# Performance work log

Measured on AMD Instinct MI355X. Metric: run time of the kernel, lower is better.

The kernel has to match this reference:

```python
import jax, jax.numpy as jnp
import numpy as np

L, T, F = 16, 262144, 2
N = 524288
HIDDEN, OUT = 64, 3
_b = np.exp((np.log(64.0) - np.log(16.0)) / (L - 1))
# per-level resolutions: floor(N_min * b**l), kept as float for the scale multiply
N_VALUES = np.floor(np.float32(16.0 * _b ** np.arange(L))).astype(np.float32)


def setup_inputs() -> dict:
    key = jax.random.key(0)
    ks = jax.random.split(key, 6)
    X = jax.random.uniform(ks[0], (N, 2), jnp.float32)
    hash_table = jax.random.uniform(ks[1], (L, T, F), jnp.float32, minval=-1e-4, maxval=1e-4)

    def lin(k, fan_in, fan_out):
        kw, kb = jax.random.split(k)
        bound = 1.0 / np.sqrt(fan_in)
        W = jax.random.uniform(kw, (fan_in, fan_out), jnp.float32, minval=-bound, maxval=bound)
        b = jax.random.uniform(kb, (fan_out,), jnp.float32, minval=-bound, maxval=bound)
        return W, b

    W1, b1 = lin(ks[2], L * F, HIDDEN)
    W2, b2 = lin(ks[3], HIDDEN, HIDDEN)
    W3, b3 = lin(ks[4], HIDDEN, HIDDEN)
    W4, b4 = lin(ks[5], HIDDEN, OUT)
    return dict(X=X, hash_table=hash_table, W1=W1, b1=b1, W2=W2, b2=b2,
                W3=W3, b3=b3, W4=W4, b4=b4)


def _encode(X, hash_table):
    nvals = jnp.asarray(N_VALUES)
    x_scaled = X[:, :, None] * nvals                      # [N,2,L]
    frac = x_scaled - jnp.floor(x_scaled)                 # [N,2,L]
    vertices = jnp.array([[0., 0., 1., 1.], [0., 1., 0., 1.]], jnp.float32)  # [2,4]
    # faithful to source: scaled coord * vertex mask (not floor + offset), then int truncation
    x_vert = (x_scaled[:, :, :, None] * vertices[None, :, None, :]).astype(jnp.uint32)  # [N,2,L,4]
    primes = jnp.array([1, 2654435761], dtype=jnp.uint32)
    xt = x_vert * primes[None, :, None, None]
    # source takes xor then mod 2 (not mod T); LSB is exact under uint32 wraparound
    x_hash = (jnp.bitwise_xor(xt[:, 0], xt[:, 1]) % 2).astype(jnp.int32)  # [N,L,4] in {0,1}
    xp = jnp.transpose(x_hash, (1, 0, 2))                 # [L,N,4]
    # faithful to source's torch.gather along dim 0: out[l,n,k,f] = table[hash, k, f]
    lookup = hash_table[xp, jnp.arange(4)[None, None, :], :]  # [L,N,4,F]
    lookup = jnp.transpose(lookup, (1, 0, 2, 3))          # [N,L,4,F]
    fx, fy = frac[:, 0, :], frac[:, 1, :]
    cx, cy = 1.0 - fx, 1.0 - fy
    f_stack = jnp.stack([cx * cy, cx * fy, fx * cy, fx * fy], axis=2)  # [N,L,4]
    x_interp = jnp.einsum('nlv,nlvf->nlf', f_stack, lookup)           # [N,L,F]
    return x_interp.reshape(-1, L * F)


def reference(X, hash_table, W1, b1, W2, b2, W3, b3, W4, b4):
    h = _encode(X, hash_table)
    lrelu = lambda z: jnp.where(z >= 0, z, 0.01 * z)  # LeakyReLU default slope
    h = lrelu(h @ W1 + b1)
    h = lrelu(h @ W2 + b2)
    h = lrelu(h @ W3 + b3)
    return jax.nn.relu(h @ W4 + b4)
```

## Files before the change

### kernel.cpp

```cpp
#include <hip/hip_runtime.h>


typedef float  f32x4  __attribute__((ext_vector_type(4)));
typedef __bf16 bf16x8 __attribute__((ext_vector_type(8)));

#define MFMA16(A, B, C) __builtin_amdgcn_mfma_f32_16x16x32_bf16((A), (B), (C), 0, 0, 0)

__global__ __launch_bounds__(256) void hashnerf_mfma(
    const float* __restrict__ X,
    const float* __restrict__ HT,
    const float* __restrict__ W1, const float* __restrict__ B1,
    const float* __restrict__ W2, const float* __restrict__ B2,
    const float* __restrict__ W3, const float* __restrict__ B3,
    const float* __restrict__ W4, const float* __restrict__ B4,
    float* __restrict__ out, int npts)
{
    __shared__ __align__(16) float sBias[208];
    __shared__ __align__(16) float sH[4][16 * 68];

    const int tid = threadIdx.x;
    if (tid < 64) {
        sBias[tid]       = B1[tid];
        sBias[64 + tid]  = B2[tid];
        sBias[128 + tid] = B3[tid];
    }
    if (tid < 16) sBias[192 + tid] = (tid < 3) ? B4[tid] : 0.0f;
    __syncthreads();

    const int l  = tid & 63;
    const int p  = l & 15;
    const int g  = l >> 4;
    const int wv = tid >> 6;
    float* __restrict__ Hw = sH[wv];

    bf16x8 w1h[4];
#pragma unroll
    for (int t = 0; t < 4; ++t) {
#pragma unroll
        for (int e = 0; e < 8; ++e) {
            float w = W1[(8 * g + e) * 64 + p + 16 * t];
            w1h[t][e] = (__bf16)w;
        }
    }
    bf16x8 w2h[4][2], w2l[4][2], w3h[4][2], w3l[4][2];
#pragma unroll
    for (int t = 0; t < 4; ++t) {
#pragma unroll
        for (int s = 0; s < 2; ++s) {
#pragma unroll
            for (int e = 0; e < 8; ++e) {
                float w2 = W2[(32 * s + 8 * g + e) * 64 + p + 16 * t];
                __bf16 h2 = (__bf16)w2;
                w2h[t][s][e] = h2; w2l[t][s][e] = (__bf16)(w2 - (float)h2);
                float w3 = W3[(32 * s + 8 * g + e) * 64 + p + 16 * t];
                __bf16 h3 = (__bf16)w3;
                w3h[t][s][e] = h3; w3l[t][s][e] = (__bf16)(w3 - (float)h3);
            }
        }
    }
    bf16x8 w4h[2], w4l[2];
#pragma unroll
    for (int s = 0; s < 2; ++s) {
#pragma unroll
        for (int e = 0; e < 8; ++e) {
            float w = (p < 3) ? W4[(32 * s + 8 * g + e) * 3 + p] : 0.0f;
            __bf16 h = (__bf16)w;
            w4h[s][e] = h; w4l[s][e] = (__bf16)(w - (float)h);
        }
    }

    float t0[8], t1[8];
#pragma unroll
    for (int e = 0; e < 8; ++e) { t0[e] = HT[e]; t1[e] = HT[524288 + e]; }

    const float NVA[4] = {16.f, 17.f, 19.f, 21.f};
    const float NVB[4] = {23.f, 25.f, 27.f, 30.f};
    const float NVC[4] = {33.f, 36.f, 40.f, 44.f};
    const float NVD[4] = {48.f, 53.f, 58.f, 64.f};
    float nv4[4];
#pragma unroll
    for (int j = 0; j < 4; ++j)
        nv4[j] = (g == 0) ? NVA[j] : (g == 1) ? NVB[j] : (g == 2) ? NVC[j] : NVD[j];

    auto mlp_layer = [&](const bf16x8 (&wh)[4][2], const bf16x8 (&wl)[4][2],
                         const float* __restrict__ bofs) {
        f32x4 a2[4];
#pragma unroll
        for (int t = 0; t < 4; ++t)
            a2[t] = *reinterpret_cast<const f32x4*>(&bofs[16 * t + 4 * g]);
#pragma unroll
        for (int s = 0; s < 2; ++s) {
            f32x4 q0 = *reinterpret_cast<const f32x4*>(&Hw[p * 68 + 32 * s + 8 * g]);
            f32x4 q1 = *reinterpret_cast<const f32x4*>(&Hw[p * 68 + 32 * s + 8 * g + 4]);
            bf16x8 xh, xl;
#pragma unroll
            for (int e = 0; e < 4; ++e) {
                __bf16 h0 = (__bf16)q0[e];
                xh[e] = h0;     xl[e] = (__bf16)(q0[e] - (float)h0);
                __bf16 h1 = (__bf16)q1[e];
                xh[4 + e] = h1; xl[4 + e] = (__bf16)(q1[e] - (float)h1);
            }
#pragma unroll
            for (int t = 0; t < 4; ++t) {
                a2[t] = MFMA16(wh[t][s], xh, a2[t]);
                a2[t] = MFMA16(wh[t][s], xl, a2[t]);
                a2[t] = MFMA16(wl[t][s], xh, a2[t]);
            }
        }
#pragma unroll
        for (int t = 0; t < 4; ++t) {
            f32x4 v = a2[t];
#pragma unroll
            for (int r = 0; r < 4; ++r) v[r] = fmaxf(v[r], 0.01f * v[r]);
            *reinterpret_cast<f32x4*>(&Hw[p * 68 + 16 * t + 4 * g]) = v;
        }
    };

    const int wave_global = blockIdx.x * 4 + wv;
    const int nwaves = gridDim.x * 4;
    const int ntiles = (npts + 15) >> 4;
    const float2* X2 = reinterpret_cast<const float2*>(X);

    for (int tile = wave_global; tile < ntiles; tile += nwaves) {
        const int pbase = tile << 4;
        const int pidx  = min(pbase + p, npts - 1);
        const float2 xv = X2[pidx];

        bf16x8 bh;
#pragma unroll
        for (int j2 = 0; j2 < 4; ++j2) {
            const float nv = nv4[j2];
            const float sx = xv.x * nv, sy = xv.y * nv;
            const float fx = sx - floorf(sx), fy = sy - floorf(sy);
            const unsigned ix = (unsigned)sx, iy = (unsigned)sy;
            const bool px = (ix & 1u) != 0u, py = (iy & 1u) != 0u;
            const bool pz = px != py;
            const float cx = 1.f - fx, cy = 1.f - fy;
            const float q0 = cx * cy, q1 = cx * fy, q2 = fx * cy, q3 = fx * fy;
            float a0 = q0 * t0[0];
            a0 = fmaf(q1, py ? t1[2] : t0[2], a0);
            a0 = fmaf(q2, px ? t1[4] : t0[4], a0);
            a0 = fmaf(q3, pz ? t1[6] : t0[6], a0);
            float a1 = q0 * t0[1];
            a1 = fmaf(q1, py ? t1[3] : t0[3], a1);
            a1 = fmaf(q2, px ? t1[5] : t0[5], a1);
            a1 = fmaf(q3, pz ? t1[7] : t0[7], a1);
            bh[2 * j2]     = (__bf16)a0;
            bh[2 * j2 + 1] = (__bf16)a1;
        }

        f32x4 acc[4];
#pragma unroll
        for (int t = 0; t < 4; ++t) {
            acc[t] = *reinterpret_cast<const f32x4*>(&sBias[16 * t + 4 * g]);
            acc[t] = MFMA16(w1h[t], bh, acc[t]);
        }
#pragma unroll
        for (int t = 0; t < 4; ++t) {
            f32x4 v = acc[t];
#pragma unroll
            for (int r = 0; r < 4; ++r) v[r] = fmaxf(v[r], 0.01f * v[r]);
            *reinterpret_cast<f32x4*>(&Hw[p * 68 + 16 * t + 4 * g]) = v;
        }

        mlp_layer(w2h, w2l, &sBias[64]);
        mlp_layer(w3h, w3l, &sBias[128]);

        f32x4 ao = *reinterpret_cast<const f32x4*>(&sBias[192 + 4 * g]);
#pragma unroll
        for (int s = 0; s < 2; ++s) {
            f32x4 q0 = *reinterpret_cast<const f32x4*>(&Hw[p * 68 + 32 * s + 8 * g]);
            f32x4 q1 = *reinterpret_cast<const f32x4*>(&Hw[p * 68 + 32 * s + 8 * g + 4]);
            bf16x8 xh, xl;
#pragma unroll
            for (int e = 0; e < 4; ++e) {
                __bf16 h0 = (__bf16)q0[e];
                xh[e] = h0;     xl[e] = (__bf16)(q0[e] - (float)h0);
                __bf16 h1 = (__bf16)q1[e];
                xh[4 + e] = h1; xl[4 + e] = (__bf16)(q1[e] - (float)h1);
            }
            ao = MFMA16(w4h[s], xh, ao);
            ao = MFMA16(w4h[s], xl, ao);
            ao = MFMA16(w4l[s], xh, ao);
        }
        if (g == 0 && pbase + p < npts) {
            float* op = out + (size_t)(pbase + p) * 3;
            op[0] = fmaxf(ao[0], 0.0f);
            op[1] = fmaxf(ao[1], 0.0f);
            op[2] = fmaxf(ao[2], 0.0f);
        }
    }
}

extern "C" void kernel_launch(void* const* d_in, const int* in_sizes, int n_in,
                              void* d_out, int out_size, void* d_ws, size_t ws_size,
                              hipStream_t stream) {
    const float* X  = (const float*)d_in[0];
    const float* HT = (const float*)d_in[1];
    const float* W1 = (const float*)d_in[2];
    const float* B1 = (const float*)d_in[3];
    const float* W2 = (const float*)d_in[4];
    const float* B2 = (const float*)d_in[5];
    const float* W3 = (const float*)d_in[6];
    const float* B3 = (const float*)d_in[7];
    const float* W4 = (const float*)d_in[8];
    const float* B4 = (const float*)d_in[9];
    float* out = (float*)d_out;

    const int npts = in_sizes[0] / 2;
    hipLaunchKernelGGL(hashnerf_mfma, dim3(512), dim3(256), 0, stream,
                       X, HT, W1, B1, W2, B2, W3, B3, W4, B4, out, npts);
}
```

Measured before the change: 155.1 us.

## Store hidden activations as split bf16 hi/lo in LDS, prefetch X, raise occupancy

Hidden activations are now written to shared memory already split into bf16 high and low parts, so each consumer reads two bf16x8 vectors directly. Previously each layer reloaded fp32 values and redid the split conversion. The next tile's X coordinates are prefetched one iteration ahead to hide global load latency. Launch bounds now request 3 blocks per CU and the grid grows to 768 blocks, which raises occupancy but may force register spilling given the large register-resident weight arrays.

```diff
diff --git a/kernel.cpp b/kernel.cpp
--- a/kernel.cpp
+++ b/kernel.cpp
@@ -2,11 +2,12 @@
 
 
 typedef float  f32x4  __attribute__((ext_vector_type(4)));
+typedef __bf16 bf16x4 __attribute__((ext_vector_type(4)));
 typedef __bf16 bf16x8 __attribute__((ext_vector_type(8)));
 
 #define MFMA16(A, B, C) __builtin_amdgcn_mfma_f32_16x16x32_bf16((A), (B), (C), 0, 0, 0)
 
-__global__ __launch_bounds__(256) void hashnerf_mfma(
+__global__ __launch_bounds__(256, 3) void hashnerf_mfma(
     const float* __restrict__ X,
     const float* __restrict__ HT,
     const float* __restrict__ W1, const float* __restrict__ B1,
@@ -15,8 +16,9 @@
     const float* __restrict__ W4, const float* __restrict__ B4,
     float* __restrict__ out, int npts)
 {
-    __shared__ __align__(16) float sBias[208];
-    __shared__ __align__(16) float sH[4][16 * 68];
+    __shared__ __align__(16) float  sBias[208];
+    __shared__ __align__(16) __bf16 sHh[4][16 * 72];
+    __shared__ __align__(16) __bf16 sHl[4][16 * 72];
 
     const int tid = threadIdx.x;
     if (tid < 64) {
@@ -31,22 +33,21 @@
     const int p  = l & 15;
     const int g  = l >> 4;
     const int wv = tid >> 6;
-    float* __restrict__ Hw = sH[wv];
+    __bf16* __restrict__ Hh = sHh[wv];
+    __bf16* __restrict__ Hl = sHl[wv];
 
     bf16x8 w1h[4];
 #pragma unroll
-    for (int t = 0; t < 4; ++t) {
-#pragma unroll
-        for (int e = 0; e < 8; ++e) {
-            float w = W1[(8 * g + e) * 64 + p + 16 * t];
-            w1h[t][e] = (__bf16)w;
-        }
-    }
+    for (int t = 0; t < 4; ++t)
+#pragma unroll
+        for (int e = 0; e < 8; ++e)
+            w1h[t][e] = (__bf16)W1[(8 * g + e) * 64 + p + 16 * t];
+
     bf16x8 w2h[4][2], w2l[4][2], w3h[4][2], w3l[4][2];
 #pragma unroll
-    for (int t = 0; t < 4; ++t) {
-#pragma unroll
-        for (int s = 0; s < 2; ++s) {
+    for (int t = 0; t < 4; ++t)
+#pragma unroll
+        for (int s = 0; s < 2; ++s)
 #pragma unroll
             for (int e = 0; e < 8; ++e) {
                 float w2 = W2[(32 * s + 8 * g + e) * 64 + p + 16 * t];
@@ -56,18 +57,16 @@
                 __bf16 h3 = (__bf16)w3;
                 w3h[t][s][e] = h3; w3l[t][s][e] = (__bf16)(w3 - (float)h3);
             }
-        }
-    }
+
     bf16x8 w4h[2], w4l[2];
 #pragma unroll
-    for (int s = 0; s < 2; ++s) {
+    for (int s = 0; s < 2; ++s)
 #pragma unroll
         for (int e = 0; e < 8; ++e) {
             float w = (p < 3) ? W4[(32 * s + 8 * g + e) * 3 + p] : 0.0f;
             __bf16 h = (__bf16)w;
             w4h[s][e] = h; w4l[s][e] = (__bf16)(w - (float)h);
         }
-    }
 
     float t0[8], t1[8];
 #pragma unroll
@@ -90,16 +89,8 @@
             a2[t] = *reinterpret_cast<const f32x4*>(&bofs[16 * t + 4 * g]);
 #pragma unroll
         for (int s = 0; s < 2; ++s) {
-            f32x4 q0 = *reinterpret_cast<const f32x4*>(&Hw[p * 68 + 32 * s + 8 * g]);
-            f32x4 q1 = *reinterpret_cast<const f32x4*>(&Hw[p * 68 + 32 * s + 8 * g + 4]);
-            bf16x8 xh, xl;
-#pragma unroll
-            for (int e = 0; e < 4; ++e) {
-                __bf16 h0 = (__bf16)q0[e];
-                xh[e] = h0;     xl[e] = (__bf16)(q0[e] - (float)h0);
-                __bf16 h1 = (__bf16)q1[e];
-                xh[4 + e] = h1; xl[4 + e] = (__bf16)(q1[e] - (float)h1);
-            }
+            bf16x8 xh = *reinterpret_cast<const bf16x8*>(&Hh[p * 72 + 32 * s + 8 * g]);
+            bf16x8 xl = *reinterpret_cast<const bf16x8*>(&Hl[p * 72 + 32 * s + 8 * g]);
 #pragma unroll
             for (int t = 0; t < 4; ++t) {
                 a2[t] = MFMA16(wh[t][s], xh, a2[t]);
@@ -110,9 +101,16 @@
 #pragma unroll
         for (int t = 0; t < 4; ++t) {
             f32x4 v = a2[t];
-#pragma unroll
-            for (int r = 0; r < 4; ++r) v[r] = fmaxf(v[r], 0.01f * v[r]);
-            *reinterpret_cast<f32x4*>(&Hw[p * 68 + 16 * t + 4 * g]) = v;
+            bf16x4 hv, lv;
+#pragma unroll
+            for (int r = 0; r < 4; ++r) {
+                v[r] = fmaxf(v[r], 0.01f * v[r]);
+                __bf16 h = (__bf16)v[r];
+                hv[r] = h;
+                lv[r] = (__bf16)(v[r] - (float)h);
+            }
+            *reinterpret_cast<bf16x4*>(&Hh[p * 72 + 16 * t + 4 * g]) = hv;
+            *reinterpret_cast<bf16x4*>(&Hl[p * 72 + 16 * t + 4 * g]) = lv;
         }
     };
 
@@ -121,10 +119,14 @@
     const int ntiles = (npts + 15) >> 4;
     const float2* X2 = reinterpret_cast<const float2*>(X);
 
-    for (int tile = wave_global; tile < ntiles; tile += nwaves) {
-        const int pbase = tile << 4;
-        const int pidx  = min(pbase + p, npts - 1);
-        const float2 xv = X2[pidx];
+    int tile = wave_global;
+    float2 xv = make_float2(0.f, 0.f);
+    if (tile < ntiles) xv = X2[min(tile * 16 + p, npts - 1)];
+
+    for (; tile < ntiles; tile += nwaves) {
+        const int nt = tile + nwaves;
+        float2 xnext = xv;
+        if (nt < ntiles) xnext = X2[min(nt * 16 + p, npts - 1)];
 
         bf16x8 bh;
 #pragma unroll
@@ -158,9 +160,16 @@
 #pragma unroll
         for (int t = 0; t < 4; ++t) {
             f32x4 v = acc[t];
-#pragma unroll
-            for (int r = 0; r < 4; ++r) v[r] = fmaxf(v[r], 0.01f * v[r]);
-            *reinterpret_cast<f32x4*>(&Hw[p * 68 + 16 * t + 4 * g]) = v;
+            bf16x4 hv, lv;
+#pragma unroll
+            for (int r = 0; r < 4; ++r) {
+                v[r] = fmaxf(v[r], 0.01f * v[r]);
+                __bf16 h = (__bf16)v[r];
+                hv[r] = h;
+                lv[r] = (__bf16)(v[r] - (float)h);
+            }
+            *reinterpret_cast<bf16x4*>(&Hh[p * 72 + 16 * t + 4 * g]) = hv;
+            *reinterpret_cast<bf16x4*>(&Hl[p * 72 + 16 * t + 4 * g]) = lv;
         }
 
         mlp_layer(w2h, w2l, &sBias[64]);
@@ -169,26 +178,20 @@
         f32x4 ao = *reinterpret_cast<const f32x4*>(&sBias[192 + 4 * g]);
 #pragma unroll
         for (int s = 0; s < 2; ++s) {
-            f32x4 q0 = *reinterpret_cast<const f32x4*>(&Hw[p * 68 + 32 * s + 8 * g]);
-            f32x4 q1 = *reinterpret_cast<const f32x4*>(&Hw[p * 68 + 32 * s + 8 * g + 4]);
-            bf16x8 xh, xl;
-#pragma unroll
-            for (int e = 0; e < 4; ++e) {
-                __bf16 h0 = (__bf16)q0[e];
-                xh[e] = h0;     xl[e] = (__bf16)(q0[e] - (float)h0);
-                __bf16 h1 = (__bf16)q1[e];
-                xh[4 + e] = h1; xl[4 + e] = (__bf16)(q1[e] - (float)h1);
-            }
+            bf16x8 xh = *reinterpret_cast<const bf16x8*>(&Hh[p * 72 + 32 * s + 8 * g]);
+            bf16x8 xl = *reinterpret_cast<const bf16x8*>(&Hl[p * 72 + 32 * s + 8 * g]);
             ao = MFMA16(w4h[s], xh, ao);
             ao = MFMA16(w4h[s], xl, ao);
             ao = MFMA16(w4l[s], xh, ao);
         }
-        if (g == 0 && pbase + p < npts) {
-            float* op = out + (size_t)(pbase + p) * 3;
+        if (g == 0 && tile * 16 + p < npts) {
+            float* op = out + (size_t)(tile * 16 + p) * 3;
             op[0] = fmaxf(ao[0], 0.0f);
             op[1] = fmaxf(ao[1], 0.0f);
             op[2] = fmaxf(ao[2], 0.0f);
         }
+
+        xv = xnext;
     }
 }
 
@@ -208,6 +211,6 @@
     float* out = (float*)d_out;
 
     const int npts = in_sizes[0] / 2;
-    hipLaunchKernelGGL(hashnerf_mfma, dim3(512), dim3(256), 0, stream,
+    hipLaunchKernelGGL(hashnerf_mfma, dim3(768), dim3(256), 0, stream,
                        X, HT, W1, B1, W2, B2, W3, B3, W4, B4, out, npts);
 }
```

Result: slower. 233.3 us (+50.5%).
